# Performance work log

Measured on AMD Instinct MI355X. Metric: run time of the kernel, lower is better.

Reference implementation:

```python
import jax, jax.numpy as jnp
import numpy as np

KERNEL_SIZE = 16
STRIDE = 8
NEG = -1.0e9


def setup_inputs() -> dict:
    key = jax.random.key(0)
    k1, k2, k3, k4, k5 = jax.random.split(key, 5)
    B, C, L = 8, 512, 4096
    x = jax.random.normal(k1, (B, C, L), dtype=jnp.float32)
    mask = jax.random.randint(k2, (B, L), 0, 2).astype(bool)
    W = jax.random.normal(k3, (C, C), dtype=jnp.float32) * 0.02
    b = jax.random.normal(k4, (C,), dtype=jnp.float32) * 0.02
    v = jax.random.normal(k5, (C,), dtype=jnp.float32) * 0.02
    return {"x": x, "mask": mask, "W": W, "b": b, "v": v}


def reference(x, mask, W, b, v):
    # x: [B, C, L], mask: [B, L] (True = masked out)
    B, C, L = x.shape
    win, step = KERNEL_SIZE, STRIDE
    L_pool = 1 + (L - win) // step
    # per-token projection (identical across windows since proj is per-token)
    h = jnp.tanh(jnp.einsum('bcl,dc->bld', x, W) + b)      # [B, L, C]
    s = jnp.einsum('bld,d->bl', h, v)                       # [B, L]
    idx = jnp.arange(L_pool)[:, None] * step + jnp.arange(win)[None, :]
    sw = s[:, idx]
    mw = mask[:, idx]
    sw = jnp.where(mw, NEG, sw)
    w = jax.nn.softmax(sw, axis=-1)
    w = jnp.where(mw, 0.0, w)
    norm = jnp.clip(jnp.sum(w, axis=-1, keepdims=True), 1e-6, None)
    w = w / norm
    xw = x[:, :, idx]
    return jnp.einsum('bcpw,bpw->bcp', xw, w)               # [B, C, L_pool]
```

## Files before the change

kernel.cpp:

```cpp
#include <hip/hip_runtime.h>
#include <hip/hip_bf16.h>
#include <cmath>

#define Bsz 8
#define Csz 512
#define Lsz 4096
#define LPOOL 511
#define NEGV -1000000000.0f

typedef __attribute__((ext_vector_type(8))) short short8;
typedef __attribute__((ext_vector_type(4))) float float4v;

__device__ __forceinline__ float bf2f(short u) {
  unsigned int x = ((unsigned int)(unsigned short)u) << 16;
  return __builtin_bit_cast(float, x);
}

__device__ __forceinline__ float ftanh(float x) {
  float e = __expf(2.0f * x);
  return 1.0f - 2.0f * __builtin_amdgcn_rcpf(e + 1.0f);
}

__device__ __forceinline__ void gl_lds16(const __hip_bfloat16* g, void* l) {
  __builtin_amdgcn_global_load_lds(
      (const __attribute__((address_space(1))) unsigned int*)g,
      (__attribute__((address_space(3))) unsigned int*)l, 16, 0, 0);
}

__global__ __launch_bounds__(256) void prep(const unsigned char* __restrict__ mb,
    int* __restrict__ flag, const float* __restrict__ W,
    __hip_bfloat16* __restrict__ Wts) {
  const int tid = threadIdx.x;
  const int pb = blockIdx.x;
  if (pb == 0) {
    __shared__ int sf;
    if (tid == 0) sf = 0;
    __syncthreads();
    int f = 0;
    for (int i = tid; i < 4096; i += 256)
      if ((i & 3) && mb[i]) f = 1;
    if (f) atomicOr(&sf, 1);
    __syncthreads();
    if (tid == 0) *flag = sf;
  } else {
    int tg = (pb - 1) * 256 + tid;
    int d = tg >> 6, cg = tg & 63;
    float4 w0 = *(const float4*)(W + (size_t)d * 512 + cg * 8);
    float4 w1 = *(const float4*)(W + (size_t)d * 512 + cg * 8 + 4);
    __hip_bfloat16 hb[8];
    hb[0] = __float2bfloat16(w0.x); hb[1] = __float2bfloat16(w0.y);
    hb[2] = __float2bfloat16(w0.z); hb[3] = __float2bfloat16(w0.w);
    hb[4] = __float2bfloat16(w1.x); hb[5] = __float2bfloat16(w1.y);
    hb[6] = __float2bfloat16(w1.z); hb[7] = __float2bfloat16(w1.w);
    int nt = d >> 7, row = d & 127, ks = cg >> 2, seg = cg & 3;
    *(short8*)(Wts + (((size_t)nt * 16 + ks) * 512 + seg * 128 + row) * 8) = *(short8*)hb;
  }
}

__global__ __launch_bounds__(256, 2) void gemm_fused(
    const float* __restrict__ x, const __hip_bfloat16* __restrict__ Wts,
    const float* __restrict__ bias, const float* __restrict__ v,
    float* __restrict__ s, __hip_bfloat16* __restrict__ xbf) {
  __shared__ short8 sA[4096];
  __shared__ __align__(16) char sPool[16384];

  const int tid = threadIdx.x;
  const int lane = tid & 63, wave = tid >> 6;
  const int mt = blockIdx.x;
  const int b = mt >> 6;
  const int l0 = (mt & 63) << 6;

  {
    float* sXw = (float*)sPool + wave * 544;
    const int r = lane >> 1;
    const int q = lane & 1;
    const size_t rowbase =
        (((size_t)(b * Csz + r)) << 12) + (size_t)(l0 + wave * 16 + q * 8);
    const float* xg = x + rowbase;
    const int ll = lane & 15, kseg = lane >> 4;

    float4 a0 = *(const float4*)(xg);
    float4 a1 = *(const float4*)(xg + 4);
    float4 b0 = *(const float4*)(xg + (1u << 17));
    float4 b1 = *(const float4*)(xg + (1u << 17) + 4);
    float4 c0 = a0, c1 = a1;

    for (int cc = 0; cc < 16; ++cc) {
      if (cc < 14) {
        const float* xn = xg + ((size_t)(cc + 2) << 17);
        c0 = *(const float4*)(xn);
        c1 = *(const float4*)(xn + 4);
      }
      __hip_bfloat16 hb[8];
      hb[0] = __float2bfloat16(a0.x); hb[1] = __float2bfloat16(a0.y);
      hb[2] = __float2bfloat16(a0.z); hb[3] = __float2bfloat16(a0.w);
      hb[4] = __float2bfloat16(a1.x); hb[5] = __float2bfloat16(a1.y);
      hb[6] = __float2bfloat16(a1.z); hb[7] = __float2bfloat16(a1.w);
      *(short8*)(xbf + rowbase + ((size_t)cc << 17)) = *(short8*)hb;
      *(float4*)(&sXw[r * 17 + q * 8])     = a0;
      *(float4*)(&sXw[r * 17 + q * 8 + 4]) = a1;
      asm volatile("s_waitcnt lgkmcnt(0)" ::: "memory");
      __builtin_amdgcn_sched_barrier(0);
      float tv[8];
      #pragma unroll
      for (int j = 0; j < 8; ++j) tv[j] = sXw[(kseg * 8 + j) * 17 + ll];
      __hip_bfloat16 ab[8];
      #pragma unroll
      for (int j = 0; j < 8; ++j) ab[j] = __float2bfloat16(tv[j]);
      sA[(cc * 4 + kseg) * 64 + wave * 16 + ll] = *(short8*)ab;
      asm volatile("s_waitcnt lgkmcnt(0)" ::: "memory");
      __builtin_amdgcn_sched_barrier(0);
      a0 = b0; a1 = b1; b0 = c0; b1 = c1;
    }
  }

  const int lr = lane & 15, quad = lane >> 4;
  const int mh = wave >> 1, nh = wave & 1;

  float bl[4][4], vl[4][4];
  #pragma unroll
  for (int nt = 0; nt < 4; ++nt)
    #pragma unroll
    for (int nf = 0; nf < 4; ++nf) {
      int n = nt * 128 + nh * 64 + nf * 16 + lr;
      bl[nt][nf] = bias[n];
      vl[nt][nf] = v[n];
    }

  __syncthreads();
  short8 (*sB)[512] = (short8 (*)[512])sPool;
  {
    const __hip_bfloat16* gb = Wts + (size_t)(wave * 64 + lane) * 8;
    gl_lds16(gb,        &sB[0][wave * 64]);
    gl_lds16(gb + 2048, &sB[0][256 + wave * 64]);
  }
  __syncthreads();

  float sp[2][4];
  #pragma unroll
  for (int mf = 0; mf < 2; ++mf)
    #pragma unroll
    for (int reg = 0; reg < 4; ++reg) sp[mf][reg] = 0.f;

  #pragma unroll
  for (int nt = 0; nt < 4; ++nt) {
    float4v acc[2][4];
    #pragma unroll
    for (int mf = 0; mf < 2; ++mf)
      #pragma unroll
      for (int nf = 0; nf < 4; ++nf) acc[mf][nf] = (float4v)0.f;

    #pragma unroll 2
    for (int ks = 0; ks < 16; ++ks) {
      const int idx = nt * 16 + ks;
      const int cur = idx & 1;
      if (idx < 63) {
        const __hip_bfloat16* gb =
            Wts + ((size_t)(idx + 1) << 12) + (size_t)(wave * 64 + lane) * 8;
        gl_lds16(gb,        &sB[cur ^ 1][wave * 64]);
        gl_lds16(gb + 2048, &sB[cur ^ 1][256 + wave * 64]);
        asm volatile("s_waitcnt vmcnt(2)" ::: "memory");
      } else {
        asm volatile("s_waitcnt vmcnt(0)" ::: "memory");
      }
      __builtin_amdgcn_sched_barrier(0);
      __builtin_amdgcn_s_barrier();
      short8 af[2], bfr[4];
      #pragma unroll
      for (int mf = 0; mf < 2; ++mf)
        af[mf] = sA[(ks * 4 + quad) * 64 + mh * 32 + mf * 16 + lr];
      #pragma unroll
      for (int nf = 0; nf < 4; ++nf)
        bfr[nf] = sB[cur][quad * 128 + nh * 64 + nf * 16 + lr];
      __builtin_amdgcn_s_setprio(1);
      #pragma unroll
      for (int mf = 0; mf < 2; ++mf)
        #pragma unroll
        for (int nf = 0; nf < 4; ++nf)
          acc[mf][nf] = __builtin_amdgcn_mfma_f32_16x16x32_bf16(
              af[mf], bfr[nf], acc[mf][nf], 0, 0, 0);
      __builtin_amdgcn_s_setprio(0);
      __builtin_amdgcn_s_barrier();
    }
    #pragma unroll
    for (int mf = 0; mf < 2; ++mf)
      #pragma unroll
      for (int reg = 0; reg < 4; ++reg) {
        float pp = 0.f;
        #pragma unroll
        for (int nf = 0; nf < 4; ++nf)
          pp += ftanh(acc[mf][nf][reg] + bl[nt][nf]) * vl[nt][nf];
        sp[mf][reg] += pp;
      }
  }

  float* sRed = (float*)sPool;
  float pv[2][4];
  #pragma unroll
  for (int mf = 0; mf < 2; ++mf)
    #pragma unroll
    for (int reg = 0; reg < 4; ++reg) {
      float p = sp[mf][reg];
      p += __shfl_xor(p, 1, 16);
      p += __shfl_xor(p, 2, 16);
      p += __shfl_xor(p, 4, 16);
      p += __shfl_xor(p, 8, 16);
      pv[mf][reg] = p;
    }
  if (nh == 1 && lr == 0) {
    #pragma unroll
    for (int mf = 0; mf < 2; ++mf)
      #pragma unroll
      for (int reg = 0; reg < 4; ++reg)
        sRed[((mh * 2 + mf) * 4 + quad) * 4 + reg] = pv[mf][reg];
  }
  __syncthreads();
  if (nh == 0 && lr == 0) {
    #pragma unroll
    for (int mf = 0; mf < 2; ++mf)
      #pragma unroll
      for (int reg = 0; reg < 4; ++reg)
        s[mt * 64 + mh * 32 + mf * 16 + quad * 4 + reg] =
            pv[mf][reg] + sRed[((mh * 2 + mf) * 4 + quad) * 4 + reg];
  }
}

__global__ __launch_bounds__(256) void pool2(const __hip_bfloat16* __restrict__ xbf,
    const float* __restrict__ s, const void* __restrict__ mask,
    const int* __restrict__ flag, float* __restrict__ out) {
  __shared__ float wl[8][17];
  const int t = threadIdx.x;
  const int p0 = blockIdx.x * 8, b = blockIdx.y;
  const int ch = blockIdx.z;
  if (t < 8 && p0 + t < LPOOL) {
    const int p = p0 + t;
    const bool u8 = (*flag != 0);
    const unsigned char* m8 = (const unsigned char*)mask;
    const int* m32 = (const int*)mask;
    const int base = b * Lsz + p * 8;
    float sv[16]; int mv[16];
    float mx = -3.4e38f;
    #pragma unroll
    for (int w = 0; w < 16; ++w) {
      int mk = u8 ? (int)m8[base + w] : m32[base + w];
      float val = mk ? NEGV : s[base + w];
      sv[w] = val; mv[w] = mk;
      mx = fmaxf(mx, val);
    }
    float sum = 0.f;
    #pragma unroll
    for (int w = 0; w < 16; ++w) { sv[w] = expf(sv[w] - mx); sum += sv[w]; }
    float inv = 1.0f / sum;
    float norm = 0.f;
    #pragma unroll
    for (int w = 0; w < 16; ++w) { sv[w] = mv[w] ? 0.f : sv[w] * inv; norm += sv[w]; }
    norm = fmaxf(norm, 1e-6f);
    float rn = 1.0f / norm;
    #pragma unroll
    for (int w = 0; w < 16; ++w) wl[t][w] = sv[w] * rn;
  }
  __syncthreads();
  const int ci = t >> 3, pi = t & 7;
  const int p = p0 + pi;
  if (p >= LPOOL) return;
  float wr[16];
  #pragma unroll
  for (int w = 0; w < 16; ++w) wr[w] = wl[pi][w];
  #pragma unroll
  for (int it = 0; it < 8; ++it) {
    int c = ch * 256 + it * 32 + ci;
    const __hip_bfloat16* xp = xbf + ((size_t)b * Csz + c) * Lsz + 8 * p;
    short8 lo = *(const short8*)xp;
    short8 hi = *(const short8*)(xp + 8);
    float acc = 0.f;
    #pragma unroll
    for (int j = 0; j < 8; ++j)
      acc += bf2f(lo[j]) * wr[j] + bf2f(hi[j]) * wr[8 + j];
    out[((size_t)b * Csz + c) * LPOOL + p] = acc;
  }
}

__global__ void detect_mask(const unsigned char* __restrict__ mb, int* __restrict__ flag) {
  __shared__ int sf;
  int t = threadIdx.x;
  if (t == 0) sf = 0;
  __syncthreads();
  int f = 0;
  for (int i = t; i < 4096; i += 256)
    if ((i & 3) && mb[i]) f = 1;
  if (f) atomicOr(&sf, 1);
  __syncthreads();
  if (t == 0) *flag = sf;
}

__global__ __launch_bounds__(256) void gemm_s_f32(const float* __restrict__ x,
    const float* __restrict__ W, const float* __restrict__ bias,
    const float* __restrict__ v, float* __restrict__ s_out) {
  __shared__ float sA[32][64];
  __shared__ float sB[32][68];
  __shared__ float s_acc[64];
  const int tid = threadIdx.x;
  const int b = blockIdx.y;
  const int l0 = blockIdx.x * 64;
  if (tid < 64) s_acc[tid] = 0.0f;
  const int tx = tid & 15;
  const int ty = tid >> 4;
  const float* xb = x + ((size_t)b * Csz) * Lsz + l0;
  for (int d0 = 0; d0 < Csz; d0 += 64) {
    float acc[4][4] = {{0.f}};
    for (int c0 = 0; c0 < Csz; c0 += 32) {
      __syncthreads();
      #pragma unroll
      for (int it = 0; it < 8; ++it) {
        int idx = tid + it * 256;
        int kc = idx >> 6, ml = idx & 63;
        sA[kc][ml] = xb[(size_t)(c0 + kc) * Lsz + ml];
      }
      #pragma unroll
      for (int it = 0; it < 8; ++it) {
        int idx = tid + it * 256;
        int kc = idx & 31, dj = idx >> 5;
        sB[kc][dj] = W[(size_t)(d0 + dj) * Csz + c0 + kc];
      }
      __syncthreads();
      #pragma unroll
      for (int kc = 0; kc < 32; ++kc) {
        float4 a  = *(const float4*)(&sA[kc][tx << 2]);
        float4 w4 = *(const float4*)(&sB[kc][ty << 2]);
        acc[0][0] += a.x * w4.x; acc[0][1] += a.x * w4.y; acc[0][2] += a.x * w4.z; acc[0][3] += a.x * w4.w;
        acc[1][0] += a.y * w4.x; acc[1][1] += a.y * w4.y; acc[1][2] += a.y * w4.z; acc[1][3] += a.y * w4.w;
        acc[2][0] += a.z * w4.x; acc[2][1] += a.z * w4.y; acc[2][2] += a.z * w4.z; acc[2][3] += a.z * w4.w;
        acc[3][0] += a.w * w4.x; acc[3][1] += a.w * w4.y; acc[3][2] += a.w * w4.z; acc[3][3] += a.w * w4.w;
      }
    }
    float part[4] = {0.f, 0.f, 0.f, 0.f};
    #pragma unroll
    for (int j = 0; j < 4; ++j) {
      int d = d0 + (ty << 2) + j;
      float bj = bias[d], vj = v[d];
      #pragma unroll
      for (int i = 0; i < 4; ++i)
        part[i] += tanhf(acc[i][j] + bj) * vj;
    }
    #pragma unroll
    for (int i = 0; i < 4; ++i)
      atomicAdd(&s_acc[(tx << 2) + i], part[i]);
  }
  __syncthreads();
  if (tid < 64) s_out[(size_t)b * Lsz + l0 + tid] = s_acc[tid];
}

__global__ void win_weights(const float* __restrict__ s, const void* __restrict__ mask,
                            const int* __restrict__ flag, float* __restrict__ wgt) {
  int t = blockIdx.x * blockDim.x + threadIdx.x;
  if (t >= Bsz * LPOOL) return;
  int b = t / LPOOL, p = t - b * LPOOL;
  const bool u8 = (*flag != 0);
  const unsigned char* m8 = (const unsigned char*)mask;
  const int* m32 = (const int*)mask;
  float sv[16]; int mv[16];
  float mx = -3.4e38f;
  int base = b * Lsz + p * 8;
  #pragma unroll
  for (int w = 0; w < 16; ++w) {
    int mk = u8 ? (int)m8[base + w] : m32[base + w];
    float val = mk ? NEGV : s[base + w];
    sv[w] = val; mv[w] = mk;
    mx = fmaxf(mx, val);
  }
  float sum = 0.f;
  #pragma unroll
  for (int w = 0; w < 16; ++w) { sv[w] = expf(sv[w] - mx); sum += sv[w]; }
  float inv = 1.0f / sum;
  float norm = 0.f;
  #pragma unroll
  for (int w = 0; w < 16; ++w) { sv[w] = mv[w] ? 0.f : sv[w] * inv; norm += sv[w]; }
  norm = fmaxf(norm, 1e-6f);
  float rn = 1.0f / norm;
  #pragma unroll
  for (int w = 0; w < 16; ++w) wgt[t * 16 + w] = sv[w] * rn;
}

__global__ __launch_bounds__(256) void pool_out(const float* __restrict__ x,
    const float* __restrict__ wgt, float* __restrict__ out) {
  __shared__ float xrow[Lsz];
  int bc = blockIdx.x;
  int c = bc & (Csz - 1);
  int b = bc >> 9;
  const float* xr = x + ((size_t)b * Csz + c) * Lsz;
  int tid = threadIdx.x;
  #pragma unroll
  for (int it = 0; it < 4; ++it) {
    int idx = (tid + it * 256) << 2;
    *(float4*)(&xrow[idx]) = *(const float4*)(&xr[idx]);
  }
  __syncthreads();
  const float* wb = wgt + (size_t)b * LPOOL * 16;
  float* ob = out + ((size_t)b * Csz + c) * LPOOL;
  for (int p = tid; p < LPOOL; p += 256) {
    const float4* wp = (const float4*)(wb + p * 16);
    const float4* xp = (const float4*)(&xrow[p * 8]);
    float acc = 0.f;
    #pragma unroll
    for (int q = 0; q < 4; ++q) {
      float4 wv = wp[q], xv = xp[q];
      acc += xv.x * wv.x + xv.y * wv.y + xv.z * wv.z + xv.w * wv.w;
    }
    ob[p] = acc;
  }
}

extern "C" void kernel_launch(void* const* d_in, const int* in_sizes, int n_in,
                              void* d_out, int out_size, void* d_ws, size_t ws_size,
                              hipStream_t stream) {
  const float* x    = (const float*)d_in[0];
  const void*  mask = d_in[1];
  const float* W    = (const float*)d_in[2];
  const float* bias = (const float*)d_in[3];
  const float* v    = (const float*)d_in[4];
  float* out = (float*)d_out;

  char* wsb = (char*)d_ws;
  int*   flag = (int*)wsb;
  float* s    = (float*)(wsb + 256);
  float* wgt  = (float*)(wsb + 131328);
  __hip_bfloat16* Wts = (__hip_bfloat16*)(wsb + 393216);
  __hip_bfloat16* xbf = (__hip_bfloat16*)(wsb + 917504);
  const size_t NEED = 917504 + 33554432;

  if (ws_size >= NEED) {
    prep<<<129, 256, 0, stream>>>((const unsigned char*)mask, flag, W, Wts);
    gemm_fused<<<512, 256, 0, stream>>>(x, Wts, bias, v, s, xbf);
    pool2<<<dim3(64, Bsz, 2), 256, 0, stream>>>(xbf, s, mask, flag, out);
  } else {
    detect_mask<<<1, 256, 0, stream>>>((const unsigned char*)mask, flag);
    gemm_s_f32<<<dim3(Lsz / 64, Bsz), 256, 0, stream>>>(x, W, bias, v, s);
    win_weights<<<(Bsz * LPOOL + 255) / 256, 256, 0, stream>>>(s, mask, flag, wgt);
    pool_out<<<Bsz * Csz, 256, 0, stream>>>(x, wgt, out);
  }
}
```

Before: 159.7 us.

## Drop bf16 x copy; pool reads fp32 x, GEMM stages x via async LDS pipeline

The GEMM kernel no longer writes a 32 MB bf16 copy of x. The pooling kernel now reads the original fp32 x directly. The x tile load in the GEMM is rewritten as a 5-buffer global_load_lds pipeline with vmcnt waits and barriers, and launch bounds drop to 1 block per SM because the shared memory footprint grows. The aim is to remove the extra write traffic, in exchange for pool reading twice as many bytes and lower GEMM occupancy.

```diff
diff --git a/kernel.cpp b/kernel.cpp
--- a/kernel.cpp
+++ b/kernel.cpp
@@ -21,7 +21,7 @@
   return 1.0f - 2.0f * __builtin_amdgcn_rcpf(e + 1.0f);
 }
 
-__device__ __forceinline__ void gl_lds16(const __hip_bfloat16* g, void* l) {
+__device__ __forceinline__ void gl_lds16(const void* g, void* l) {
   __builtin_amdgcn_global_load_lds(
       (const __attribute__((address_space(1))) unsigned int*)g,
       (__attribute__((address_space(3))) unsigned int*)l, 16, 0, 0);
@@ -57,12 +57,12 @@
   }
 }
 
-__global__ __launch_bounds__(256, 2) void gemm_fused(
+__global__ __launch_bounds__(256, 1) void gemm_fused(
     const float* __restrict__ x, const __hip_bfloat16* __restrict__ Wts,
     const float* __restrict__ bias, const float* __restrict__ v,
-    float* __restrict__ s, __hip_bfloat16* __restrict__ xbf) {
+    float* __restrict__ s) {
   __shared__ short8 sA[4096];
-  __shared__ __align__(16) char sPool[16384];
+  __shared__ __align__(16) float sXs[5][2048];
 
   const int tid = threadIdx.x;
   const int lane = tid & 63, wave = tid >> 6;
@@ -70,53 +70,42 @@
   const int b = mt >> 6;
   const int l0 = (mt & 63) << 6;
 
+  const int quad = lane >> 4, sub = lane & 15;
+  const int lr = lane & 15;
+
   {
-    float* sXw = (float*)sPool + wave * 544;
-    const int r = lane >> 1;
-    const int q = lane & 1;
-    const size_t rowbase =
-        (((size_t)(b * Csz + r)) << 12) + (size_t)(l0 + wave * 16 + q * 8);
-    const float* xg = x + rowbase;
-    const int ll = lane & 15, kseg = lane >> 4;
-
-    float4 a0 = *(const float4*)(xg);
-    float4 a1 = *(const float4*)(xg + 4);
-    float4 b0 = *(const float4*)(xg + (1u << 17));
-    float4 b1 = *(const float4*)(xg + (1u << 17) + 4);
-    float4 c0 = a0, c1 = a1;
-
-    for (int cc = 0; cc < 16; ++cc) {
-      if (cc < 14) {
-        const float* xn = xg + ((size_t)(cc + 2) << 17);
-        c0 = *(const float4*)(xn);
-        c1 = *(const float4*)(xn + 4);
-      }
-      __hip_bfloat16 hb[8];
-      hb[0] = __float2bfloat16(a0.x); hb[1] = __float2bfloat16(a0.y);
-      hb[2] = __float2bfloat16(a0.z); hb[3] = __float2bfloat16(a0.w);
-      hb[4] = __float2bfloat16(a1.x); hb[5] = __float2bfloat16(a1.y);
-      hb[6] = __float2bfloat16(a1.z); hb[7] = __float2bfloat16(a1.w);
-      *(short8*)(xbf + rowbase + ((size_t)cc << 17)) = *(short8*)hb;
-      *(float4*)(&sXw[r * 17 + q * 8])     = a0;
-      *(float4*)(&sXw[r * 17 + q * 8 + 4]) = a1;
-      asm volatile("s_waitcnt lgkmcnt(0)" ::: "memory");
-      __builtin_amdgcn_sched_barrier(0);
+    const float* xb = x + (size_t)(b * Csz) * Lsz + l0;
+#define ISSUE_CHUNK(k)                                                         \
+  {                                                                            \
+    const float* g0 = xb + (size_t)((k) * 32 + wave * 8 + quad) * Lsz + sub * 4; \
+    gl_lds16(g0,           &sXs[(k) % 5][(wave * 8) * 64]);                    \
+    gl_lds16(g0 + 4 * Lsz, &sXs[(k) % 5][(wave * 8 + 4) * 64]);                \
+  }
+    ISSUE_CHUNK(0)
+    ISSUE_CHUNK(1)
+    ISSUE_CHUNK(2)
+    #pragma unroll
+    for (int k = 0; k < 16; ++k) {
+      if (k + 3 < 16) ISSUE_CHUNK(k + 3)
+      if (k < 13)       asm volatile("s_waitcnt vmcnt(6)" ::: "memory");
+      else if (k == 13) asm volatile("s_waitcnt vmcnt(4)" ::: "memory");
+      else if (k == 14) asm volatile("s_waitcnt vmcnt(2)" ::: "memory");
+      else              asm volatile("s_waitcnt vmcnt(0)" ::: "memory");
+      __builtin_amdgcn_s_barrier();
+      const float* bufp = &sXs[k % 5][0];
       float tv[8];
       #pragma unroll
-      for (int j = 0; j < 8; ++j) tv[j] = sXw[(kseg * 8 + j) * 17 + ll];
+      for (int j = 0; j < 8; ++j) tv[j] = bufp[(quad * 8 + j) * 64 + wave * 16 + sub];
       __hip_bfloat16 ab[8];
       #pragma unroll
       for (int j = 0; j < 8; ++j) ab[j] = __float2bfloat16(tv[j]);
-      sA[(cc * 4 + kseg) * 64 + wave * 16 + ll] = *(short8*)ab;
-      asm volatile("s_waitcnt lgkmcnt(0)" ::: "memory");
-      __builtin_amdgcn_sched_barrier(0);
-      a0 = b0; a1 = b1; b0 = c0; b1 = c1;
-    }
-  }
-
-  const int lr = lane & 15, quad = lane >> 4;
+      sA[(k * 4 + quad) * 64 + wave * 16 + sub] = *(short8*)ab;
+    }
+#undef ISSUE_CHUNK
+    __builtin_amdgcn_sched_barrier(0);
+  }
+
   const int mh = wave >> 1, nh = wave & 1;
-
   float bl[4][4], vl[4][4];
   #pragma unroll
   for (int nt = 0; nt < 4; ++nt)
@@ -128,7 +117,7 @@
     }
 
   __syncthreads();
-  short8 (*sB)[512] = (short8 (*)[512])sPool;
+  short8 (*sB)[512] = (short8 (*)[512])sXs;
   {
     const __hip_bfloat16* gb = Wts + (size_t)(wave * 64 + lane) * 8;
     gl_lds16(gb,        &sB[0][wave * 64]);
@@ -194,7 +183,7 @@
       }
   }
 
-  float* sRed = (float*)sPool;
+  float* sRed = (float*)sXs + 4096;
   float pv[2][4];
   #pragma unroll
   for (int mf = 0; mf < 2; ++mf)
@@ -225,7 +214,7 @@
   }
 }
 
-__global__ __launch_bounds__(256) void pool2(const __hip_bfloat16* __restrict__ xbf,
+__global__ __launch_bounds__(256) void pool2(const float* __restrict__ x,
     const float* __restrict__ s, const void* __restrict__ mask,
     const int* __restrict__ flag, float* __restrict__ out) {
   __shared__ float wl[8][17];
@@ -269,13 +258,15 @@
   #pragma unroll
   for (int it = 0; it < 8; ++it) {
     int c = ch * 256 + it * 32 + ci;
-    const __hip_bfloat16* xp = xbf + ((size_t)b * Csz + c) * Lsz + 8 * p;
-    short8 lo = *(const short8*)xp;
-    short8 hi = *(const short8*)(xp + 8);
-    float acc = 0.f;
-    #pragma unroll
-    for (int j = 0; j < 8; ++j)
-      acc += bf2f(lo[j]) * wr[j] + bf2f(hi[j]) * wr[8 + j];
+    const float* xp = x + ((size_t)b * Csz + c) * Lsz + 8 * p;
+    float4 x0 = *(const float4*)(xp);
+    float4 x1 = *(const float4*)(xp + 4);
+    float4 x2 = *(const float4*)(xp + 8);
+    float4 x3 = *(const float4*)(xp + 12);
+    float acc = x0.x * wr[0] + x0.y * wr[1] + x0.z * wr[2] + x0.w * wr[3]
+              + x1.x * wr[4] + x1.y * wr[5] + x1.z * wr[6] + x1.w * wr[7]
+              + x2.x * wr[8] + x2.y * wr[9] + x2.z * wr[10] + x2.w * wr[11]
+              + x3.x * wr[12] + x3.y * wr[13] + x3.z * wr[14] + x3.w * wr[15];
     out[((size_t)b * Csz + c) * LPOOL + p] = acc;
   }
 }
@@ -425,13 +416,12 @@
   float* s    = (float*)(wsb + 256);
   float* wgt  = (float*)(wsb + 131328);
   __hip_bfloat16* Wts = (__hip_bfloat16*)(wsb + 393216);
-  __hip_bfloat16* xbf = (__hip_bfloat16*)(wsb + 917504);
-  const size_t NEED = 917504 + 33554432;
+  const size_t NEED = 917504;
 
   if (ws_size >= NEED) {
     prep<<<129, 256, 0, stream>>>((const unsigned char*)mask, flag, W, Wts);
-    gemm_fused<<<512, 256, 0, stream>>>(x, Wts, bias, v, s, xbf);
-    pool2<<<dim3(64, Bsz, 2), 256, 0, stream>>>(xbf, s, mask, flag, out);
+    gemm_fused<<<512, 256, 0, stream>>>(x, Wts, bias, v, s);
+    pool2<<<dim3(64, Bsz, 2), 256, 0, stream>>>(x, s, mask, flag, out);
   } else {
     detect_mask<<<1, 256, 0, stream>>>((const unsigned char*)mask, flag);
     gemm_s_f32<<<dim3(Lsz / 64, Bsz), 256, 0, stream>>>(x, W, bias, v, s);
```

Measured after the change: 185.7 us. 16.3% more time.
